# Optimization experiments

Hardware: AMD Instinct MI355X
Metric: run time of the kernel (lower is better)

The kernel has to match this reference:

```python
import jax, jax.numpy as jnp
import numpy as np
from jax import lax

B, C, H, W = 16, 256, 128, 128
MAX_ROOMS = 10

def _conv(x, w, b):
    y = lax.conv_general_dilated(x, w, window_strides=(1, 1), padding='SAME',
                                 dimension_numbers=('NCHW', 'OIHW', 'NCHW'))
    return y + b[None, :, None, None]

def setup_inputs() -> dict:
    key = jax.random.key(0)
    ks = jax.random.split(key, 16)
    def w(k, shape, fan_in):
        return jax.random.normal(k, shape, jnp.float32) * (1.0 / np.sqrt(fan_in))
    inp = {
        'features': jax.random.normal(ks[0], (B, C, H, W), jnp.float32),
        'conv1_w': w(ks[1], (C // 2, C, 3, 3), C * 9),
        'conv1_b': jnp.zeros((C // 2,), jnp.float32),
        'conv2_w': w(ks[2], (MAX_ROOMS, C // 2, 3, 3), (C // 2) * 9),
        'conv2_b': jnp.zeros((MAX_ROOMS,), jnp.float32),
        'lin1_w': w(ks[3], (256, C * 64), C * 64),
        'lin1_b': jnp.zeros((256,), jnp.float32),
        'lin2_w': w(ks[4], (128, 256), 256),
        'lin2_b': jnp.zeros((128,), jnp.float32),
        'adj1_w': w(ks[5], (64, 256), 256),
        'adj1_b': jnp.zeros((64,), jnp.float32),
        'adj2_w': w(ks[6], (32, 64), 64),
        'adj2_b': jnp.zeros((32,), jnp.float32),
        'adj3_w': w(ks[7], (1, 32), 32),
        'adj3_b': jnp.zeros((1,), jnp.float32),
    }
    return inp

def reference(features, conv1_w, conv1_b, conv2_w, conv2_b,
              lin1_w, lin1_b, lin2_w, lin2_b,
              adj1_w, adj1_b, adj2_w, adj2_b, adj3_w, adj3_b):
    # room detector: conv -> relu -> conv -> sigmoid
    h = jax.nn.relu(_conv(features, conv1_w, conv1_b))
    room_maps = jax.nn.sigmoid(_conv(h, conv2_w, conv2_b))  # [B, max_rooms, H, W]

    # room features: adaptive avg pool to 8x8 (exact since H,W divisible by 8)
    b, c = features.shape[0], features.shape[1]
    pooled = features.reshape(b, c, 8, H // 8, 8, W // 8).mean(axis=(3, 5))  # [B,C,8,8]
    flat = pooled.reshape(b, c * 64)
    feat = jax.nn.relu(flat @ lin1_w.T + lin1_b) @ lin2_w.T + lin2_b  # [B,128]

    # adjacency: original loop uses the SAME pair_feat=cat([feat,feat]) for every (i,j),
    # so compute one prob per batch row and broadcast to all off-diagonal entries.
    pair = jnp.concatenate([feat, feat], axis=-1)  # [B,256]
    a = jax.nn.relu(pair @ adj1_w.T + adj1_b)
    a = jax.nn.relu(a @ adj2_w.T + adj2_b)
    p = jax.nn.sigmoid(a @ adj3_w.T + adj3_b)  # [B,1]
    off_diag = 1.0 - jnp.eye(MAX_ROOMS, dtype=features.dtype)
    adjacency = p[:, :, None] * off_diag[None]  # [B, max_rooms, max_rooms]

    return room_maps, feat, adjacency
```

## Files before the change

kernel.cpp:

```cpp
#include <hip/hip_runtime.h>

#define HH 128
#define WW 128
#define FEAT_OFF 2621440ull
#define ADJ_OFF  2623488ull

typedef __bf16 bf16x8 __attribute__((ext_vector_type(8)));
typedef float  f32x4  __attribute__((ext_vector_type(4)));
typedef float  f32x16 __attribute__((ext_vector_type(16)));

__device__ __forceinline__ unsigned short f2bf(float f) {
  unsigned int u = __float_as_uint(f);
  unsigned int r = ((u >> 16) & 1u) + 0x7fffu;
  return (unsigned short)((u + r) >> 16);
}
__device__ __forceinline__ void gl_lds16(const void* g, void* l) {
  __builtin_amdgcn_global_load_lds((const __attribute__((address_space(1))) unsigned int*)g,
                                   (__attribute__((address_space(3))) unsigned int*)l, 16, 0, 0);
}
__device__ __forceinline__ int SW(int r) { return (r ^ (r >> 2)) & 3; }

#define FENCE() asm volatile("" ::: "memory")
#define BARRIER() do { FENCE(); __builtin_amdgcn_s_barrier(); FENCE(); } while (0)
#define LBAR() do { asm volatile("s_waitcnt lgkmcnt(0)" ::: "memory"); __builtin_amdgcn_s_barrier(); FENCE(); } while (0)

__global__ void prep_kernel(const float* __restrict__ w1, const float* __restrict__ w2,
                            unsigned short* __restrict__ W1t, unsigned short* __restrict__ W2t,
                            unsigned short* __restrict__ zp) {
  int id = blockIdx.x * 256 + threadIdx.x;
  if (id < 2048) zp[id] = 0;
  if (id < 294912) {
    int ci = id & 255, co = (id >> 8) & 127, dxy = id >> 15;
    int dy = dxy / 3, dx = dxy - 3 * dy;
    W1t[id] = f2bf(w1[((co * 256 + ci) * 3 + dy) * 3 + dx]);
  }
  if (id < 18432) {
    int ci = id & 127, co = (id >> 7) & 15, dxy = id >> 11;
    int dy = dxy / 3, dx = dxy - 3 * dy;
    W2t[id] = (co < 10) ? f2bf(w2[((co * 128 + ci) * 3 + dy) * 3 + dx]) : (unsigned short)0;
  }
}

__global__ void nhwc_kernel(const float* __restrict__ F, unsigned short* __restrict__ Xn,
                            float* __restrict__ part) {
  __shared__ __align__(16) unsigned short tile[16384];
  __shared__ float pl[1024];
  int t = threadIdx.x, bi = blockIdx.x;
  int chalf = bi & 1, y = (bi >> 1) & 127, b = bi >> 8;
  int c0 = chalf * 128;
  int cp = t >> 2, xq = t & 3;
  const float* rowA = F + (((size_t)(b * 256 + c0 + cp * 2)) * HH + y) * WW + xq * 32;
  const float* rowB = rowA + (size_t)HH * WW;
  unsigned int* tw = (unsigned int*)tile;
  float s00 = 0.f, s01 = 0.f, s10 = 0.f, s11 = 0.f;
#pragma unroll
  for (int jj = 0; jj < 8; ++jj) {
    float4 va = *(const float4*)(rowA + jj * 4);
    float4 vb = *(const float4*)(rowB + jj * 4);
    float av[4] = {va.x, va.y, va.z, va.w};
    float bv[4] = {vb.x, vb.y, vb.z, vb.w};
#pragma unroll
    for (int e = 0; e < 4; ++e) {
      int xl = jj * 4 + e;
      int x = xq * 32 + xl;
      if (xl < 16) { s00 += av[e]; s10 += bv[e]; } else { s01 += av[e]; s11 += bv[e]; }
      unsigned int word = (unsigned int)f2bf(av[e]) | ((unsigned int)f2bf(bv[e]) << 16);
      tw[x * 64 + (((cp >> 2) ^ (x & 15)) << 2) + (cp & 3)] = word;
    }
  }
  pl[(cp * 2 + 0) * 8 + xq * 2 + 0] = s00;
  pl[(cp * 2 + 0) * 8 + xq * 2 + 1] = s01;
  pl[(cp * 2 + 1) * 8 + xq * 2 + 0] = s10;
  pl[(cp * 2 + 1) * 8 + xq * 2 + 1] = s11;
  __syncthreads();
  int x = t >> 1, h = t & 1;
  unsigned short* dst = Xn + ((((size_t)b * HH + y) * WW) + x) * 256 + c0;
#pragma unroll
  for (int k = 0; k < 8; ++k) {
    int s = h * 8 + k;
    *(uint4*)(dst + s * 8) = *(const uint4*)(tile + x * 128 + ((s ^ (x & 15)) << 3));
  }
  *(float4*)&part[((((size_t)b * 128 + y) * 2) + chalf) * 1024 + t * 4] = *(const float4*)&pl[t * 4];
}

__global__ void pool3_kernel(const float* __restrict__ part, float* __restrict__ pooled) {
  int bi = blockIdx.x, t = threadIdx.x;
  int py = bi & 7, chalf = (bi >> 3) & 1, b = bi >> 4;
#pragma unroll
  for (int q = 0; q < 4; ++q) {
    int i = q * 256 + t;
    float s = 0.f;
#pragma unroll
    for (int yy = 0; yy < 16; ++yy)
      s += part[((((size_t)b * 128 + py * 16 + yy) * 2) + chalf) * 1024 + i];
    int ch = i >> 3, px = i & 7;
    pooled[(size_t)b * 16384 + (chalf * 128 + ch) * 64 + py * 8 + px] = s * (1.f / 256.f);
  }
}

__global__ __launch_bounds__(512) void conv1_kernel(const unsigned short* __restrict__ X,
                                                    const unsigned short* __restrict__ Wt,
                                                    const float* __restrict__ bias,
                                                    unsigned short* __restrict__ Hout,
                                                    const unsigned short* __restrict__ zp) {
  extern __shared__ __align__(16) unsigned short smem[];
  const int t = threadIdx.x, l = t & 63, w = t >> 6;
  int bid = (blockIdx.x & 7) * 64 + (blockIdx.x >> 3);
  const int b = bid >> 5, y0 = (bid & 31) * 4;
  const int lane31 = l & 31, lh = l >> 5;
  const int yloc = w >> 1, xh = w & 1, xoff = xh * 64;

  f32x16 acc[2][4];
#pragma unroll
  for (int i = 0; i < 2; ++i)
#pragma unroll
    for (int j = 0; j < 4; ++j)
#pragma unroll
      for (int e = 0; e < 16; ++e) acc[i][j][e] = 0.f;

  auto issue_group = [&](int p, int i0, int i1, int bufsel) {
    int dy = p >> 3, cb = p & 7;
    unsigned short* buf = smem + bufsel * 30720;
    for (int i = i0; i < i1; ++i) {
      int c = w + 8 * i;
      if (c >= 60) break;
      const unsigned short* g;
      if (c < 36) {
        int air = c / 9, jj = c - air * 9;
        int er = jj * 16 + (l >> 2);
        int xin = er - 1;
        int row = y0 - 1 + dy + air;
        if (row >= 0 && row < HH && xin >= 0 && xin < WW && er < 130) {
          int kq = (l & 3) ^ SW(er);
          g = X + (((size_t)b * HH + row) * WW + xin) * 256 + cb * 32 + kq * 8;
        } else g = zp + l * 8;
      } else {
        int cc = c - 36;
        int dxi = cc >> 3, jj = cc & 7;
        int co = jj * 16 + (l >> 2);
        int kq = (l & 3) ^ SW(co);
        g = Wt + (((size_t)(dy * 3 + dxi)) * 128 + co) * 256 + cb * 32 + kq * 8;
      }
      gl_lds16(g, buf + c * 512);
    }
  };

  issue_group(0, 0, 8, 0);
  FENCE();
  asm volatile("s_waitcnt vmcnt(0)" ::: "memory");
  BARRIER();

  for (int p = 0; p < 24; ++p) {
    const unsigned short* buf = smem + (p & 1) * 30720;
    const unsigned short* Ab = buf + yloc * 4608;
    const unsigned short* Bb = buf + 18432;
    const int nsel = (p + 1) & 1;
#pragma unroll
    for (int dx = 0; dx < 3; ++dx) {
      if (p < 23) {
        if (dx == 0)      issue_group(p + 1, 0, 3, nsel);
        else if (dx == 1) issue_group(p + 1, 3, 6, nsel);
        else              issue_group(p + 1, 6, 8, nsel);
      }
      if (dx == 0 && p > 0) {
        FENCE();
        if (p < 23) asm volatile("s_waitcnt vmcnt(3)" ::: "memory");
        else        asm volatile("s_waitcnt vmcnt(0)" ::: "memory");
        BARRIER();
      }
      bf16x8 a[2][2], bb[4][2];
#pragma unroll
      for (int tm = 0; tm < 2; ++tm)
#pragma unroll
        for (int ks = 0; ks < 2; ++ks) {
          int er = xoff + tm * 32 + lane31 + dx;
          int slot = (ks * 2 + lh) ^ SW(er);
          a[tm][ks] = *(const bf16x8*)(Ab + er * 32 + slot * 8);
        }
#pragma unroll
      for (int tn = 0; tn < 4; ++tn)
#pragma unroll
        for (int ks = 0; ks < 2; ++ks) {
          int co = tn * 32 + lane31;
          int slot = (ks * 2 + lh) ^ SW(co);
          bb[tn][ks] = *(const bf16x8*)(Bb + dx * 4096 + co * 32 + slot * 8);
        }
      asm volatile("s_waitcnt lgkmcnt(0)" ::: "memory");
      __builtin_amdgcn_sched_barrier(0);
      __builtin_amdgcn_s_setprio(1);
#pragma unroll
      for (int ks = 0; ks < 2; ++ks)
#pragma unroll
        for (int tm = 0; tm < 2; ++tm)
#pragma unroll
          for (int tn = 0; tn < 4; ++tn)
            acc[tm][tn] = __builtin_amdgcn_mfma_f32_32x32x16_bf16(a[tm][ks], bb[tn][ks], acc[tm][tn], 0, 0, 0);
      __builtin_amdgcn_s_setprio(0);
      BARRIER();
    }
  }

  unsigned short* E = smem;
  for (int r = 0; r < 2; ++r) {
    if (xh == r) {
#pragma unroll
      for (int tn = 0; tn < 4; ++tn) {
        int co = tn * 32 + lane31;
        float bv = bias[co];
#pragma unroll
        for (int tm = 0; tm < 2; ++tm)
#pragma unroll
          for (int rr = 0; rr < 16; ++rr) {
            int row = (rr & 3) + 8 * (rr >> 2) + 4 * lh;
            int xl = tm * 32 + row;
            E[yloc * 8704 + xl * 136 + co] = f2bf(fmaxf(acc[tm][tn][rr] + bv, 0.f));
          }
      }
    }
    LBAR();
#pragma unroll
    for (int k = 0; k < 8; ++k) {
      int idx = k * 512 + t;
      int yl = idx >> 10, rem = idx & 1023;
      int xl = rem >> 4, oct = rem & 15;
      const uint4 v = *(const uint4*)(E + yl * 8704 + xl * 136 + oct * 8);
      size_t g = (((size_t)b * HH + y0 + yl) * WW + r * 64 + xl) * 128 + oct * 8;
      *(uint4*)(Hout + g) = v;
    }
    LBAR();
  }
}

__global__ __launch_bounds__(256) void conv2_kernel(const unsigned short* __restrict__ Hn,
                                                    const unsigned short* __restrict__ Wt,
                                                    const float* __restrict__ bias,
                                                    float* __restrict__ rmaps,
                                                    const unsigned short* __restrict__ zp) {
  extern __shared__ __align__(16) unsigned short smem[];
  const int t = threadIdx.x, l = t & 63, w = t >> 6;
  int bid = (blockIdx.x & 7) * 64 + (blockIdx.x >> 3);
  const int b = bid >> 5, y0 = (bid & 31) * 4;
  const int ko = l >> 4, r0 = l & 15;
  const int yloc = w;

  f32x4 acc[8];
#pragma unroll
  for (int i = 0; i < 8; ++i) acc[i] = {0.f, 0.f, 0.f, 0.f};

  auto stage = [&](int cb, int bufsel) {
    unsigned short* buf = smem + bufsel * 32256;
    for (int c = w; c < 63; c += 4) {
      const unsigned short* g;
      if (c < 54) {
        int air = c / 9, jj = c - air * 9;
        int er = jj * 16 + (l >> 2);
        int xin = er - 1;
        int row = y0 - 1 + air;
        if (row >= 0 && row < HH && xin >= 0 && xin < WW && er < 130) {
          int kq = (l & 3) ^ SW(er);
          g = Hn + (((size_t)b * HH + row) * WW + xin) * 128 + cb * 32 + kq * 8;
        } else g = zp + l * 8;
      } else {
        int tap = c - 54;
        int co = l >> 2;
        int kq = (l & 3) ^ SW(co);
        g = Wt + ((size_t)tap * 16 + co) * 128 + cb * 32 + kq * 8;
      }
      gl_lds16(g, buf + c * 512);
    }
  };

  stage(0, 0);
  for (int p = 0; p < 4; ++p) {
    if (p < 3) {
      stage(p + 1, (p + 1) & 1);
      FENCE();
      asm volatile("s_waitcnt vmcnt(15)" ::: "memory");
    } else {
      FENCE();
      asm volatile("s_waitcnt vmcnt(0)" ::: "memory");
    }
    BARRIER();
    const unsigned short* buf = smem + (p & 1) * 32256;
#pragma unroll
    for (int dy = 0; dy < 3; ++dy) {
      const unsigned short* Ab = buf + (yloc + dy) * 4608;
#pragma unroll
      for (int dx = 0; dx < 3; ++dx) {
        int tap = dy * 3 + dx;
        bf16x8 bbf = *(const bf16x8*)(buf + (54 + tap) * 512 + r0 * 32 + ((ko ^ SW(r0)) << 3));
        __builtin_amdgcn_s_setprio(1);
#pragma unroll
        for (int mf = 0; mf < 8; ++mf) {
          int er = mf * 16 + r0 + dx;
          bf16x8 a = *(const bf16x8*)(Ab + er * 32 + ((ko ^ SW(er)) << 3));
          acc[mf] = __builtin_amdgcn_mfma_f32_16x16x32_bf16(a, bbf, acc[mf], 0, 0, 0);
        }
        __builtin_amdgcn_s_setprio(0);
      }
    }
    BARRIER();
  }

  int co = r0;
  if (co < 10) {
    float bv = bias[co];
    int y = y0 + yloc;
#pragma unroll
    for (int mf = 0; mf < 8; ++mf) {
      int x = mf * 16 + ko * 4;
      float4 o;
      o.x = 1.f / (1.f + __expf(-(acc[mf][0] + bv)));
      o.y = 1.f / (1.f + __expf(-(acc[mf][1] + bv)));
      o.z = 1.f / (1.f + __expf(-(acc[mf][2] + bv)));
      o.w = 1.f / (1.f + __expf(-(acc[mf][3] + bv)));
      *(float4*)&rmaps[(((size_t)b * 10 + co) * HH + y) * WW + x] = o;
    }
  }
}

__global__ void lin1_kernel(const float* __restrict__ pooled, const float* __restrict__ w1,
                            const float* __restrict__ b1, float* __restrict__ hidden) {
  int o = blockIdx.x, t = threadIdx.x;
  float acc[16];
#pragma unroll
  for (int b = 0; b < 16; ++b) acc[b] = 0.f;
  const float* wr = w1 + (size_t)o * 16384;
  for (int i = t; i < 16384; i += 256) {
    float wv = wr[i];
#pragma unroll
    for (int b = 0; b < 16; ++b) acc[b] += wv * pooled[(size_t)b * 16384 + i];
  }
  __shared__ float red[16][4];
#pragma unroll
  for (int b = 0; b < 16; ++b) {
    float v = acc[b];
    for (int s = 32; s; s >>= 1) v += __shfl_down(v, s);
    if ((t & 63) == 0) red[b][t >> 6] = v;
  }
  __syncthreads();
  if (t < 16) {
    float v = red[t][0] + red[t][1] + red[t][2] + red[t][3] + b1[o];
    hidden[o * 16 + t] = fmaxf(v, 0.f);
  }
}

__global__ void head_kernel(const float* __restrict__ hidden,
                            const float* __restrict__ w2, const float* __restrict__ b2,
                            const float* __restrict__ a1w, const float* __restrict__ a1b,
                            const float* __restrict__ a2w, const float* __restrict__ a2b,
                            const float* __restrict__ a3w, const float* __restrict__ a3b,
                            float* __restrict__ out) {
  int b = blockIdx.x, t = threadIdx.x;
  __shared__ float hid[256], fs[128], a1[64], a2[32], pv;
  hid[t] = hidden[t * 16 + b];
  __syncthreads();
  if (t < 128) {
    float s = b2[t];
    for (int k = 0; k < 256; ++k) s += hid[k] * w2[t * 256 + k];
    fs[t] = s;
    out[FEAT_OFF + b * 128 + t] = s;
  }
  __syncthreads();
  if (t < 64) {
    float s = a1b[t];
    for (int k = 0; k < 128; ++k) s += fs[k] * (a1w[t * 256 + k] + a1w[t * 256 + 128 + k]);
    a1[t] = fmaxf(s, 0.f);
  }
  __syncthreads();
  if (t < 32) {
    float s = a2b[t];
    for (int k = 0; k < 64; ++k) s += a1[k] * a2w[t * 64 + k];
    a2[t] = fmaxf(s, 0.f);
  }
  __syncthreads();
  if (t == 0) {
    float s = a3b[0];
    for (int k = 0; k < 32; ++k) s += a2[k] * a3w[k];
    pv = 1.f / (1.f + __expf(-s));
  }
  __syncthreads();
  if (t < 100) out[ADJ_OFF + b * 100 + t] = ((t / 10) == (t % 10)) ? 0.f : pv;
}

extern "C" void kernel_launch(void* const* d_in, const int* in_sizes, int n_in,
                              void* d_out, int out_size, void* d_ws, size_t ws_size,
                              hipStream_t stream) {
  const float* F   = (const float*)d_in[0];
  const float* w1  = (const float*)d_in[1];
  const float* b1  = (const float*)d_in[2];
  const float* w2  = (const float*)d_in[3];
  const float* b2  = (const float*)d_in[4];
  const float* l1w = (const float*)d_in[5];
  const float* l1b = (const float*)d_in[6];
  const float* l2w = (const float*)d_in[7];
  const float* l2b = (const float*)d_in[8];
  const float* a1w = (const float*)d_in[9];
  const float* a1b = (const float*)d_in[10];
  const float* a2w = (const float*)d_in[11];
  const float* a2b = (const float*)d_in[12];
  const float* a3w = (const float*)d_in[13];
  const float* a3b = (const float*)d_in[14];
  float* out = (float*)d_out;
  char* ws = (char*)d_ws;

  const size_t zp_off   = 0;
  const size_t w1t_off  = 4096;
  const size_t w2t_off  = w1t_off + 589824;
  const size_t xn_off   = w2t_off + 36864;
  const size_t hn_off   = xn_off + 134217728ull;
  const size_t pool_off = hn_off + 67108864ull;
  const size_t hid_off  = pool_off + 1048576ull;
  const size_t need     = hid_off + 16384ull;
  if (ws_size < need) return;

  unsigned short* zp  = (unsigned short*)(ws + zp_off);
  unsigned short* W1t = (unsigned short*)(ws + w1t_off);
  unsigned short* W2t = (unsigned short*)(ws + w2t_off);
  unsigned short* Xn  = (unsigned short*)(ws + xn_off);
  unsigned short* Hn  = (unsigned short*)(ws + hn_off);
  float* part   = (float*)(ws + hn_off);
  float* pooled = (float*)(ws + pool_off);
  float* hidden = (float*)(ws + hid_off);

  hipFuncSetAttribute((const void*)conv1_kernel, hipFuncAttributeMaxDynamicSharedMemorySize, 122880);
  hipFuncSetAttribute((const void*)conv2_kernel, hipFuncAttributeMaxDynamicSharedMemorySize, 129024);

  prep_kernel<<<1152, 256, 0, stream>>>(w1, w2, W1t, W2t, zp);
  nhwc_kernel<<<4096, 256, 0, stream>>>(F, Xn, part);
  pool3_kernel<<<256, 256, 0, stream>>>(part, pooled);
  conv1_kernel<<<512, 512, 122880, stream>>>(Xn, W1t, b1, Hn, zp);
  conv2_kernel<<<512, 256, 129024, stream>>>(Hn, W2t, b2, out, zp);
  lin1_kernel<<<256, 256, 0, stream>>>(pooled, l1w, l1b, hidden);
  head_kernel<<<16, 256, 0, stream>>>(hidden, l2w, l2b, a1w, a1b, a2w, a2b, a3w, a3b, out);
}
```

Baseline: 373.0 us.

## Merge NHWC channel halves per block and cut conv1 per-tap barriers

The NHWC transpose kernel now handles all 256 channels of a row in a 512-thread block with dynamic LDS, so each pixel writes one contiguous 512-byte run. Pool3 is adjusted to the new partial-sum layout. In conv1 the per-dx barrier and explicit lgkmcnt wait/sched_barrier are removed, leaving one barrier before and one after the three dx steps of each stage. This trades fewer synchronisations and more compiler freedom for a risk that prefetch writes into the other buffer race with reads, and lower occupancy in the transpose.

```diff
diff --git a/kernel.cpp b/kernel.cpp
--- a/kernel.cpp
+++ b/kernel.cpp
@@ -43,15 +43,14 @@
 
 __global__ void nhwc_kernel(const float* __restrict__ F, unsigned short* __restrict__ Xn,
                             float* __restrict__ part) {
-  __shared__ __align__(16) unsigned short tile[16384];
-  __shared__ float pl[1024];
-  int t = threadIdx.x, bi = blockIdx.x;
-  int chalf = bi & 1, y = (bi >> 1) & 127, b = bi >> 8;
-  int c0 = chalf * 128;
+  extern __shared__ __align__(16) unsigned short ntile[];
+  float* pl = (float*)(ntile + 32768);
+  int t = threadIdx.x;
+  int y = blockIdx.x & 127, b = blockIdx.x >> 7;
   int cp = t >> 2, xq = t & 3;
-  const float* rowA = F + (((size_t)(b * 256 + c0 + cp * 2)) * HH + y) * WW + xq * 32;
+  const float* rowA = F + (((size_t)(b * 256 + cp * 2)) * HH + y) * WW + xq * 32;
   const float* rowB = rowA + (size_t)HH * WW;
-  unsigned int* tw = (unsigned int*)tile;
+  unsigned int* tw = (unsigned int*)ntile;
   float s00 = 0.f, s01 = 0.f, s10 = 0.f, s11 = 0.f;
 #pragma unroll
   for (int jj = 0; jj < 8; ++jj) {
@@ -65,7 +64,7 @@
       int x = xq * 32 + xl;
       if (xl < 16) { s00 += av[e]; s10 += bv[e]; } else { s01 += av[e]; s11 += bv[e]; }
       unsigned int word = (unsigned int)f2bf(av[e]) | ((unsigned int)f2bf(bv[e]) << 16);
-      tw[x * 64 + (((cp >> 2) ^ (x & 15)) << 2) + (cp & 3)] = word;
+      tw[x * 128 + (((cp >> 2) ^ (x & 15)) << 2) + (cp & 3)] = word;
     }
   }
   pl[(cp * 2 + 0) * 8 + xq * 2 + 0] = s00;
@@ -73,28 +72,31 @@
   pl[(cp * 2 + 1) * 8 + xq * 2 + 0] = s10;
   pl[(cp * 2 + 1) * 8 + xq * 2 + 1] = s11;
   __syncthreads();
-  int x = t >> 1, h = t & 1;
-  unsigned short* dst = Xn + ((((size_t)b * HH + y) * WW) + x) * 256 + c0;
-#pragma unroll
-  for (int k = 0; k < 8; ++k) {
-    int s = h * 8 + k;
-    *(uint4*)(dst + s * 8) = *(const uint4*)(tile + x * 128 + ((s ^ (x & 15)) << 3));
-  }
-  *(float4*)&part[((((size_t)b * 128 + y) * 2) + chalf) * 1024 + t * 4] = *(const float4*)&pl[t * 4];
+  {
+    int x = t >> 2, sub = t & 3;
+    unsigned short* dst = Xn + ((((size_t)b * HH + y) * WW) + x) * 256 + sub * 64;
+#pragma unroll
+    for (int k = 0; k < 8; ++k) {
+      int s = sub * 8 + k;
+      *(uint4*)(dst + k * 8) = *(const uint4*)(ntile + x * 256 + ((s ^ (x & 15)) << 3));
+    }
+  }
+  float* pd = part + ((size_t)b * 128 + y) * 2048;
+  *(float4*)&pd[t * 4] = *(const float4*)&pl[t * 4];
 }
 
 __global__ void pool3_kernel(const float* __restrict__ part, float* __restrict__ pooled) {
   int bi = blockIdx.x, t = threadIdx.x;
-  int py = bi & 7, chalf = (bi >> 3) & 1, b = bi >> 4;
-#pragma unroll
-  for (int q = 0; q < 4; ++q) {
+  int py = bi & 7, b = bi >> 3;
+#pragma unroll
+  for (int q = 0; q < 8; ++q) {
     int i = q * 256 + t;
     float s = 0.f;
 #pragma unroll
     for (int yy = 0; yy < 16; ++yy)
-      s += part[((((size_t)b * 128 + py * 16 + yy) * 2) + chalf) * 1024 + i];
-    int ch = i >> 3, px = i & 7;
-    pooled[(size_t)b * 16384 + (chalf * 128 + ch) * 64 + py * 8 + px] = s * (1.f / 256.f);
+      s += part[((size_t)b * 128 + py * 16 + yy) * 2048 + i];
+    int c = i >> 3, px = i & 7;
+    pooled[(size_t)b * 16384 + c * 64 + py * 8 + px] = s * (1.f / 256.f);
   }
 }
 
@@ -146,27 +148,24 @@
   };
 
   issue_group(0, 0, 8, 0);
-  FENCE();
-  asm volatile("s_waitcnt vmcnt(0)" ::: "memory");
-  BARRIER();
 
   for (int p = 0; p < 24; ++p) {
     const unsigned short* buf = smem + (p & 1) * 30720;
     const unsigned short* Ab = buf + yloc * 4608;
     const unsigned short* Bb = buf + 18432;
     const int nsel = (p + 1) & 1;
+
+    if (p < 23) issue_group(p + 1, 0, 3, nsel);
+    FENCE();
+    if (p < 23) asm volatile("s_waitcnt vmcnt(3)" ::: "memory");
+    else        asm volatile("s_waitcnt vmcnt(0)" ::: "memory");
+    BARRIER();
+
 #pragma unroll
     for (int dx = 0; dx < 3; ++dx) {
       if (p < 23) {
-        if (dx == 0)      issue_group(p + 1, 0, 3, nsel);
-        else if (dx == 1) issue_group(p + 1, 3, 6, nsel);
-        else              issue_group(p + 1, 6, 8, nsel);
-      }
-      if (dx == 0 && p > 0) {
-        FENCE();
-        if (p < 23) asm volatile("s_waitcnt vmcnt(3)" ::: "memory");
-        else        asm volatile("s_waitcnt vmcnt(0)" ::: "memory");
-        BARRIER();
+        if (dx == 1)      issue_group(p + 1, 3, 6, nsel);
+        else if (dx == 2) issue_group(p + 1, 6, 8, nsel);
       }
       bf16x8 a[2][2], bb[4][2];
 #pragma unroll
@@ -185,8 +184,6 @@
           int slot = (ks * 2 + lh) ^ SW(co);
           bb[tn][ks] = *(const bf16x8*)(Bb + dx * 4096 + co * 32 + slot * 8);
         }
-      asm volatile("s_waitcnt lgkmcnt(0)" ::: "memory");
-      __builtin_amdgcn_sched_barrier(0);
       __builtin_amdgcn_s_setprio(1);
 #pragma unroll
       for (int ks = 0; ks < 2; ++ks)
@@ -196,8 +193,8 @@
           for (int tn = 0; tn < 4; ++tn)
             acc[tm][tn] = __builtin_amdgcn_mfma_f32_32x32x16_bf16(a[tm][ks], bb[tn][ks], acc[tm][tn], 0, 0, 0);
       __builtin_amdgcn_s_setprio(0);
-      BARRIER();
-    }
+    }
+    BARRIER();
   }
 
   unsigned short* E = smem;
@@ -423,12 +420,13 @@
   float* pooled = (float*)(ws + pool_off);
   float* hidden = (float*)(ws + hid_off);
 
+  hipFuncSetAttribute((const void*)nhwc_kernel,  hipFuncAttributeMaxDynamicSharedMemorySize, 73728);
   hipFuncSetAttribute((const void*)conv1_kernel, hipFuncAttributeMaxDynamicSharedMemorySize, 122880);
   hipFuncSetAttribute((const void*)conv2_kernel, hipFuncAttributeMaxDynamicSharedMemorySize, 129024);
 
   prep_kernel<<<1152, 256, 0, stream>>>(w1, w2, W1t, W2t, zp);
-  nhwc_kernel<<<4096, 256, 0, stream>>>(F, Xn, part);
-  pool3_kernel<<<256, 256, 0, stream>>>(part, pooled);
+  nhwc_kernel<<<2048, 512, 73728, stream>>>(F, Xn, part);
+  pool3_kernel<<<128, 256, 0, stream>>>(part, pooled);
   conv1_kernel<<<512, 512, 122880, stream>>>(Xn, W1t, b1, Hn, zp);
   conv2_kernel<<<512, 256, 129024, stream>>>(Hn, W2t, b2, out, zp);
   lin1_kernel<<<256, 256, 0, stream>>>(pooled, l1w, l1b, hidden);
```

Measured after the change: 398.9 us. +7.0%, slower.
